# Performance work log

Hardware: AMD Instinct MI355X
Metric: run time of the kernel (lower is better)

The kernel has to match this reference:

```python
import jax, jax.numpy as jnp
import numpy as np

N_NODES = 50000


def setup_inputs() -> dict:
    key = jax.random.key(0)
    k1, k2, k3, k4 = jax.random.split(key, 4)
    in_c, hid = 256, 128
    x = jax.random.normal(k1, (N_NODES, in_c), dtype=jnp.float32)
    edge_index = jax.random.randint(k2, (2, 800000), 0, N_NODES, dtype=jnp.int32)
    # GCNConv weight (glorot) and bias
    W_conv = jax.random.normal(k3, (in_c, hid), dtype=jnp.float32) * (1.0 / np.sqrt(in_c))
    b_conv = jnp.zeros((hid,), dtype=jnp.float32)
    # Final Linear (xavier_uniform per reset_parameters)
    limit = np.sqrt(6.0 / (hid + in_c))
    W_lin = jax.random.uniform(k4, (hid, in_c), dtype=jnp.float32, minval=-limit, maxval=limit)
    b_lin = jnp.zeros((in_c,), dtype=jnp.float32)
    return {"x": x, "edge_index": edge_index, "W_conv": W_conv, "b_conv": b_conv,
            "W_lin": W_lin, "b_lin": b_lin}


def _gcn_conv(x, edge_index, W, b):
    n = x.shape[0]
    # add self-loops (standard GCN normalization)
    loop = jnp.arange(n, dtype=edge_index.dtype)
    src = jnp.concatenate([edge_index[0], loop])
    dst = jnp.concatenate([edge_index[1], loop])
    # transform first (in_c -> hid) so the edge gather moves the smaller dim
    h = x @ W  # [N, hid]
    deg = jax.ops.segment_sum(jnp.ones_like(dst, dtype=h.dtype), dst, num_segments=n)
    dinv = jnp.where(deg > 0, jax.lax.rsqrt(deg), 0.0)
    norm = dinv[src] * dinv[dst]  # [E+N]
    msg = h[src] * norm[:, None]  # [E+N, hid]
    out = jax.ops.segment_sum(msg, dst, num_segments=n)
    return out + b


def reference(x, edge_index, W_conv, b_conv, W_lin, b_lin):
    h = _gcn_conv(x, edge_index, W_conv, b_conv)  # [N, hid]
    # dropout p=0.0 -> identity
    return h @ W_lin + b_lin  # [N, in_c]
```

## Files before the change

kernel.cpp:

```cpp
#include <hip/hip_runtime.h>
#include <hip/hip_fp16.h>


#define N_NODES 50000
#define N_EDGES 800000
#define IN_C 256
#define HID 128
#define SCAN_BLOCKS ((N_NODES + 255) / 256)
#define GEMM_MBLK ((N_NODES + 63) / 64)

#define OFF_H    0UL
#define OFF_CONV 12800000UL
#define OFF_DEG  25600000UL
#define OFF_RP   25800000UL
#define OFF_DINV 26000064UL
#define OFF_RANK 26200064UL
#define OFF_REC  27800064UL
#define OFF_BSUM 31000064UL
#define OFF_WT1  31001088UL
#define OFF_WT2  31066624UL

typedef __attribute__((ext_vector_type(8))) short bf16x8;
typedef __attribute__((ext_vector_type(4))) float f32x4;

__device__ __forceinline__ ushort f2bf(float x) {
    unsigned u = __float_as_uint(x);
    u += 0x7fffu + ((u >> 16) & 1u);
    return (ushort)(u >> 16);
}

__global__ void deg_kernel(const int* __restrict__ dst, int* __restrict__ deg,
                           ushort* __restrict__ rank, int e) {
    int i = blockIdx.x * blockDim.x + threadIdx.x;
    if (i < e) rank[i] = (ushort)atomicAdd(&deg[dst[i]], 1);
}

__global__ __launch_bounds__(256) void scan_blocks_kernel(
    const int* __restrict__ deg, int* __restrict__ row_ptr,
    int* __restrict__ bsums, int n)
{
    __shared__ int tmp[256];
    int tid = threadIdx.x;
    int i = blockIdx.x * 256 + tid;
    int v = (i < n) ? deg[i] : 0;
    int orig = v;
    tmp[tid] = v;
    __syncthreads();
    #pragma unroll
    for (int off = 1; off < 256; off <<= 1) {
        int t = (tid >= off) ? tmp[tid - off] : 0;
        __syncthreads();
        tmp[tid] += t;
        __syncthreads();
    }
    if (i < n) row_ptr[i] = tmp[tid] - orig;
    if (tid == 255) bsums[blockIdx.x] = tmp[255];
}

__global__ __launch_bounds__(256) void scan_sums_kernel(int* __restrict__ bsums, int nb) {
    __shared__ int tmp[256];
    int tid = threadIdx.x;
    int v = (tid < nb) ? bsums[tid] : 0;
    int orig = v;
    tmp[tid] = v;
    __syncthreads();
    #pragma unroll
    for (int off = 1; off < 256; off <<= 1) {
        int t = (tid >= off) ? tmp[tid - off] : 0;
        __syncthreads();
        tmp[tid] += t;
        __syncthreads();
    }
    if (tid < nb) bsums[tid] = tmp[tid] - orig;
}

__global__ __launch_bounds__(256) void finalize_kernel(
    const int* __restrict__ deg, int* __restrict__ row_ptr,
    const int* __restrict__ bsums, float* __restrict__ dinv, int n)
{
    int i = blockIdx.x * 256 + threadIdx.x;
    if (i < n) {
        row_ptr[i] += bsums[blockIdx.x];
        dinv[i] = rsqrtf((float)(deg[i] + 1));
    }
    if (i == 0) row_ptr[n] = N_EDGES;
}

#define BUCKET_BLOCKS 2048
__global__ __launch_bounds__(256) void bucket_kernel(
    const int* __restrict__ src, const int* __restrict__ dst,
    const ushort* __restrict__ rank, const int* __restrict__ row_ptr,
    const float* __restrict__ dinv, unsigned* __restrict__ rec)
{
    int cls = blockIdx.x & 7;
    int blk = blockIdx.x >> 3;
    int lo = cls * (N_NODES / 8);
    int hi = lo + (N_NODES / 8);
    const int CHUNK = (N_EDGES + 255) / 256;
    int e0 = blk * CHUNK;
    int e1 = min(e0 + CHUNK, N_EDGES);
    for (int i = e0 + threadIdx.x; i < e1; i += 256) {
        int d = dst[i];
        if (d >= lo && d < hi) {
            int s = src[i];
            unsigned r = (unsigned)(ushort)s |
                         ((unsigned)__half_as_ushort(__float2half_rn(dinv[s])) << 16);
            rec[row_ptr[d] + rank[i]] = r;
        }
    }
}

__global__ void transpose_w_kernel(const float* __restrict__ W, ushort* __restrict__ Wt,
                                   int K, int N) {
    int i = blockIdx.x * 256 + threadIdx.x;
    if (i < N * K) {
        int n = i / K, k = i % K;
        Wt[i] = f2bf(W[k * N + n]);
    }
}

template <bool A_IS_BF16, bool BF16OUT>
__global__ __launch_bounds__(256) void mfma_gemm_kernel(
    const void* __restrict__ Av, const ushort* __restrict__ Bt,
    const float* __restrict__ bias, void* __restrict__ Cv,
    int M, int N, int K)
{
    constexpr int LDK = 40;
    __shared__ ushort As[64 * LDK];
    __shared__ ushort Bs[128 * LDK];
    int tid = threadIdx.x;
    int wave = tid >> 6, lane = tid & 63;
    int quad = lane >> 4, l16 = lane & 15;
    int wm0 = (wave >> 1) * 32, wn0 = (wave & 1) * 64;
    int bm = blockIdx.x * 64, bn = blockIdx.y * 128;

    f32x4 acc[2][4] = {};

    for (int k0 = 0; k0 < K; k0 += 32) {
        {
            int row = tid >> 2, col = (tid & 3) * 8;
            int grow = bm + row;
            if (A_IS_BF16) {
                bf16x8 v = {};
                if (grow < M)
                    v = *(const bf16x8*)((const ushort*)Av + (size_t)grow * K + k0 + col);
                *(bf16x8*)&As[row * LDK + col] = v;
            } else {
                float4 v0 = make_float4(0.f, 0.f, 0.f, 0.f);
                float4 v1 = make_float4(0.f, 0.f, 0.f, 0.f);
                if (grow < M) {
                    const float* ap = (const float*)Av + (size_t)grow * K + k0 + col;
                    v0 = *(const float4*)ap;
                    v1 = *(const float4*)(ap + 4);
                }
                ushort t[8] = {f2bf(v0.x), f2bf(v0.y), f2bf(v0.z), f2bf(v0.w),
                               f2bf(v1.x), f2bf(v1.y), f2bf(v1.z), f2bf(v1.w)};
                *(bf16x8*)&As[row * LDK + col] = *(bf16x8*)t;
            }
        }
        {
            int ch = tid * 2;
            int n = ch >> 2;
            int kk = (ch & 3) * 8;
            const ushort* bp = Bt + (size_t)(bn + n) * K + k0 + kk;
            *(bf16x8*)&Bs[n * LDK + kk]     = *(const bf16x8*)bp;
            *(bf16x8*)&Bs[n * LDK + kk + 8] = *(const bf16x8*)(bp + 8);
        }
        __syncthreads();
        bf16x8 af[2], bfr[4];
        #pragma unroll
        for (int im = 0; im < 2; ++im)
            af[im] = *(bf16x8*)&As[(wm0 + im * 16 + l16) * LDK + quad * 8];
        #pragma unroll
        for (int in = 0; in < 4; ++in)
            bfr[in] = *(bf16x8*)&Bs[(wn0 + in * 16 + l16) * LDK + quad * 8];
        #pragma unroll
        for (int im = 0; im < 2; ++im)
            #pragma unroll
            for (int in = 0; in < 4; ++in)
                acc[im][in] = __builtin_amdgcn_mfma_f32_16x16x32_bf16(
                    af[im], bfr[in], acc[im][in], 0, 0, 0);
        __syncthreads();
    }
    #pragma unroll
    for (int im = 0; im < 2; ++im) {
        #pragma unroll
        for (int in = 0; in < 4; ++in) {
            int col = bn + wn0 + in * 16 + l16;
            float bval = bias ? bias[col] : 0.f;
            #pragma unroll
            for (int r = 0; r < 4; ++r) {
                int grow = bm + wm0 + im * 16 + quad * 4 + r;
                if (grow < M) {
                    float o = acc[im][in][r] + bval;
                    if (BF16OUT)
                        ((ushort*)Cv)[(size_t)grow * N + col] = f2bf(o);
                    else
                        ((float*)Cv)[(size_t)grow * N + col] = o;
                }
            }
        }
    }
}

__device__ __forceinline__ void acc_edge(float4& acc, unsigned r,
                                         const ushort* __restrict__ hb, int c) {
    unsigned s = r & 0xffffu;
    float w = __half2float(__ushort_as_half((ushort)(r >> 16)));
    uint2 v = *(const uint2*)&hb[(size_t)s * HID + c];
    acc.x += w * __uint_as_float(v.x << 16);
    acc.y += w * __uint_as_float(v.x & 0xffff0000u);
    acc.z += w * __uint_as_float(v.y << 16);
    acc.w += w * __uint_as_float(v.y & 0xffff0000u);
}

__global__ __launch_bounds__(256) void gather_kernel(
    const ushort* __restrict__ hb, const int* __restrict__ row_ptr,
    const unsigned* __restrict__ rec, const float* __restrict__ dinv,
    const float* __restrict__ b_conv, ushort* __restrict__ convb, int n)
{
    int wave = threadIdx.x >> 6;
    int lane = threadIdx.x & 63;
    int d = blockIdx.x * 4 + wave;
    if (d >= n) return;
    int half = lane >> 5;
    int l32 = lane & 31;
    int c = l32 << 2;

    float4 acc = make_float4(0.f, 0.f, 0.f, 0.f);
    int begin = row_ptr[d], end = row_ptr[d + 1];
    int e = begin + half;
    for (; e + 6 < end; e += 8) {
        unsigned r0 = rec[e];
        unsigned r1 = rec[e + 2];
        unsigned r2 = rec[e + 4];
        unsigned r3 = rec[e + 6];
        acc_edge(acc, r0, hb, c);
        acc_edge(acc, r1, hb, c);
        acc_edge(acc, r2, hb, c);
        acc_edge(acc, r3, hb, c);
    }
    for (; e < end; e += 2) {
        unsigned r0 = rec[e];
        acc_edge(acc, r0, hb, c);
    }
    acc.x += __shfl_xor(acc.x, 32);
    acc.y += __shfl_xor(acc.y, 32);
    acc.z += __shfl_xor(acc.z, 32);
    acc.w += __shfl_xor(acc.w, 32);

    if (half == 0) {
        float di = dinv[d];
        uint2 hv = *(const uint2*)&hb[(size_t)d * HID + c];
        acc.x += di * __uint_as_float(hv.x << 16);
        acc.y += di * __uint_as_float(hv.x & 0xffff0000u);
        acc.z += di * __uint_as_float(hv.y << 16);
        acc.w += di * __uint_as_float(hv.y & 0xffff0000u);
        float4 bb = *(const float4*)&b_conv[c];
        float ox = di * acc.x + bb.x;
        float oy = di * acc.y + bb.y;
        float oz = di * acc.z + bb.z;
        float ow = di * acc.w + bb.w;
        uint2 po;
        po.x = ((unsigned)f2bf(oy) << 16) | (unsigned)f2bf(ox);
        po.y = ((unsigned)f2bf(ow) << 16) | (unsigned)f2bf(oz);
        *(uint2*)&convb[(size_t)d * HID + c] = po;
    }
}

extern "C" void kernel_launch(void* const* d_in, const int* in_sizes, int n_in,
                              void* d_out, int out_size, void* d_ws, size_t ws_size,
                              hipStream_t stream) {
    const float* x      = (const float*)d_in[0];
    const int*   ei     = (const int*)d_in[1];
    const float* W_conv = (const float*)d_in[2];
    const float* b_conv = (const float*)d_in[3];
    const float* W_lin  = (const float*)d_in[4];
    const float* b_lin  = (const float*)d_in[5];
    float* out = (float*)d_out;

    char* ws = (char*)d_ws;
    ushort* hb      = (ushort*)(ws + OFF_H);
    ushort* convb   = (ushort*)(ws + OFF_CONV);
    int*    deg     = (int*)(ws + OFF_DEG);
    int*    row_ptr = (int*)(ws + OFF_RP);
    float*  dinv    = (float*)(ws + OFF_DINV);
    ushort* rank    = (ushort*)(ws + OFF_RANK);
    unsigned* rec   = (unsigned*)(ws + OFF_REC);
    int*    bsums   = (int*)(ws + OFF_BSUM);
    ushort* wt_conv = (ushort*)(ws + OFF_WT1);
    ushort* wt_lin  = (ushort*)(ws + OFF_WT2);

    const int* src = ei;
    const int* dst = ei + N_EDGES;

    hipMemsetAsync(deg, 0, 200000, stream);

    deg_kernel<<<(N_EDGES + 255) / 256, 256, 0, stream>>>(dst, deg, rank, N_EDGES);
    scan_blocks_kernel<<<SCAN_BLOCKS, 256, 0, stream>>>(deg, row_ptr, bsums, N_NODES);
    scan_sums_kernel<<<1, 256, 0, stream>>>(bsums, SCAN_BLOCKS);
    finalize_kernel<<<SCAN_BLOCKS, 256, 0, stream>>>(deg, row_ptr, bsums, dinv, N_NODES);
    bucket_kernel<<<BUCKET_BLOCKS, 256, 0, stream>>>(src, dst, rank, row_ptr, dinv, rec);

    transpose_w_kernel<<<(HID * IN_C + 255) / 256, 256, 0, stream>>>(W_conv, wt_conv, IN_C, HID);
    transpose_w_kernel<<<(IN_C * HID + 255) / 256, 256, 0, stream>>>(W_lin, wt_lin, HID, IN_C);

    mfma_gemm_kernel<false, true><<<dim3(GEMM_MBLK, HID / 128), 256, 0, stream>>>(
        x, wt_conv, nullptr, hb, N_NODES, HID, IN_C);

    gather_kernel<<<(N_NODES + 3) / 4, 256, 0, stream>>>(
        hb, row_ptr, rec, dinv, b_conv, convb, N_NODES);

    mfma_gemm_kernel<true, false><<<dim3(GEMM_MBLK, IN_C / 128), 256, 0, stream>>>(
        convb, wt_lin, b_lin, out, N_NODES, IN_C, HID);
}
```

Measured before the change: 235.3 us.

## Fuse prep kernels, merge scan stages, and double GEMM K-tile to 64

Merges the degree-counting atomics with both weight transposes into one prep kernel, and folds the block-sum scan into the finalize kernel so each block rescans the block sums itself. This removes three kernel launches. The GEMM now stages a 64-wide K slice per iteration with a padded LDS stride of 72, which halves the number of loop iterations and barriers at the cost of more LDS and registers. Occupancy may drop from the larger shared tiles, and every finalize block redoes the same small scan.

```diff
diff --git a/kernel.cpp b/kernel.cpp
--- a/kernel.cpp
+++ b/kernel.cpp
@@ -8,6 +8,8 @@
 #define HID 128
 #define SCAN_BLOCKS ((N_NODES + 255) / 256)
 #define GEMM_MBLK ((N_NODES + 63) / 64)
+#define PREP_BLOCKS 1024
+#define LDK 72
 
 #define OFF_H    0UL
 #define OFF_CONV 12800000UL
@@ -29,10 +31,22 @@
     return (ushort)(u >> 16);
 }
 
-__global__ void deg_kernel(const int* __restrict__ dst, int* __restrict__ deg,
-                           ushort* __restrict__ rank, int e) {
-    int i = blockIdx.x * blockDim.x + threadIdx.x;
-    if (i < e) rank[i] = (ushort)atomicAdd(&deg[dst[i]], 1);
+__global__ __launch_bounds__(256) void prep_kernel(
+    const float* __restrict__ Wc, const float* __restrict__ Wl,
+    ushort* __restrict__ wtc, ushort* __restrict__ wtl,
+    const int* __restrict__ dst, ushort* __restrict__ rank, int* __restrict__ deg)
+{
+    int i = blockIdx.x * 256 + threadIdx.x;
+    if (i < HID * IN_C) {
+        int n = i / IN_C, k = i % IN_C;
+        wtc[i] = f2bf(Wc[k * HID + n]);
+    } else if (i < 2 * HID * IN_C) {
+        int j = i - HID * IN_C;
+        int n = j / HID, k = j % HID;
+        wtl[j] = f2bf(Wl[k * IN_C + n]);
+    }
+    for (int e = i; e < N_EDGES; e += PREP_BLOCKS * 256)
+        rank[e] = (ushort)atomicAdd(&deg[dst[e]], 1);
 }
 
 __global__ __launch_bounds__(256) void scan_blocks_kernel(
@@ -57,12 +71,16 @@
     if (tid == 255) bsums[blockIdx.x] = tmp[255];
 }
 
-__global__ __launch_bounds__(256) void scan_sums_kernel(int* __restrict__ bsums, int nb) {
+__global__ __launch_bounds__(256) void finalize2_kernel(
+    const int* __restrict__ deg, int* __restrict__ row_ptr,
+    const int* __restrict__ bsums, float* __restrict__ dinv, int n)
+{
     __shared__ int tmp[256];
+    __shared__ int orig[256];
     int tid = threadIdx.x;
-    int v = (tid < nb) ? bsums[tid] : 0;
-    int orig = v;
+    int v = (tid < SCAN_BLOCKS) ? bsums[tid] : 0;
     tmp[tid] = v;
+    orig[tid] = v;
     __syncthreads();
     #pragma unroll
     for (int off = 1; off < 256; off <<= 1) {
@@ -71,16 +89,10 @@
         tmp[tid] += t;
         __syncthreads();
     }
-    if (tid < nb) bsums[tid] = tmp[tid] - orig;
-}
-
-__global__ __launch_bounds__(256) void finalize_kernel(
-    const int* __restrict__ deg, int* __restrict__ row_ptr,
-    const int* __restrict__ bsums, float* __restrict__ dinv, int n)
-{
-    int i = blockIdx.x * 256 + threadIdx.x;
+    int boff = tmp[blockIdx.x] - orig[blockIdx.x];
+    int i = blockIdx.x * 256 + tid;
     if (i < n) {
-        row_ptr[i] += bsums[blockIdx.x];
+        row_ptr[i] += boff;
         dinv[i] = rsqrtf((float)(deg[i] + 1));
     }
     if (i == 0) row_ptr[n] = N_EDGES;
@@ -110,24 +122,14 @@
     }
 }
 
-__global__ void transpose_w_kernel(const float* __restrict__ W, ushort* __restrict__ Wt,
-                                   int K, int N) {
-    int i = blockIdx.x * 256 + threadIdx.x;
-    if (i < N * K) {
-        int n = i / K, k = i % K;
-        Wt[i] = f2bf(W[k * N + n]);
-    }
-}
-
 template <bool A_IS_BF16, bool BF16OUT>
 __global__ __launch_bounds__(256) void mfma_gemm_kernel(
     const void* __restrict__ Av, const ushort* __restrict__ Bt,
     const float* __restrict__ bias, void* __restrict__ Cv,
     int M, int N, int K)
 {
-    constexpr int LDK = 40;
-    __shared__ ushort As[64 * LDK];
-    __shared__ ushort Bs[128 * LDK];
+    __shared__ __align__(16) ushort As[64 * LDK];
+    __shared__ __align__(16) ushort Bs[128 * LDK];
     int tid = threadIdx.x;
     int wave = tid >> 6, lane = tid & 63;
     int quad = lane >> 4, l16 = lane & 15;
@@ -136,50 +138,66 @@
 
     f32x4 acc[2][4] = {};
 
-    for (int k0 = 0; k0 < K; k0 += 32) {
+    for (int k0 = 0; k0 < K; k0 += 64) {
         {
-            int row = tid >> 2, col = (tid & 3) * 8;
+            int row = tid >> 2, col = (tid & 3) * 16;
             int grow = bm + row;
             if (A_IS_BF16) {
-                bf16x8 v = {};
-                if (grow < M)
-                    v = *(const bf16x8*)((const ushort*)Av + (size_t)grow * K + k0 + col);
-                *(bf16x8*)&As[row * LDK + col] = v;
+                bf16x8 v0 = {}, v1 = {};
+                if (grow < M) {
+                    const ushort* ap = (const ushort*)Av + (size_t)grow * K + k0 + col;
+                    v0 = *(const bf16x8*)ap;
+                    v1 = *(const bf16x8*)(ap + 8);
+                }
+                *(bf16x8*)&As[row * LDK + col]     = v0;
+                *(bf16x8*)&As[row * LDK + col + 8] = v1;
             } else {
-                float4 v0 = make_float4(0.f, 0.f, 0.f, 0.f);
-                float4 v1 = make_float4(0.f, 0.f, 0.f, 0.f);
+                float4 v0 = {}, v1 = {}, v2 = {}, v3 = {};
                 if (grow < M) {
                     const float* ap = (const float*)Av + (size_t)grow * K + k0 + col;
                     v0 = *(const float4*)ap;
                     v1 = *(const float4*)(ap + 4);
+                    v2 = *(const float4*)(ap + 8);
+                    v3 = *(const float4*)(ap + 12);
                 }
-                ushort t[8] = {f2bf(v0.x), f2bf(v0.y), f2bf(v0.z), f2bf(v0.w),
-                               f2bf(v1.x), f2bf(v1.y), f2bf(v1.z), f2bf(v1.w)};
-                *(bf16x8*)&As[row * LDK + col] = *(bf16x8*)t;
+                ushort t0[8] = {f2bf(v0.x), f2bf(v0.y), f2bf(v0.z), f2bf(v0.w),
+                                f2bf(v1.x), f2bf(v1.y), f2bf(v1.z), f2bf(v1.w)};
+                ushort t1[8] = {f2bf(v2.x), f2bf(v2.y), f2bf(v2.z), f2bf(v2.w),
+                                f2bf(v3.x), f2bf(v3.y), f2bf(v3.z), f2bf(v3.w)};
+                *(bf16x8*)&As[row * LDK + col]     = *(bf16x8*)t0;
+                *(bf16x8*)&As[row * LDK + col + 8] = *(bf16x8*)t1;
             }
         }
         {
-            int ch = tid * 2;
-            int n = ch >> 2;
-            int kk = (ch & 3) * 8;
+            int n = tid >> 1;
+            int kk = (tid & 1) * 32;
             const ushort* bp = Bt + (size_t)(bn + n) * K + k0 + kk;
-            *(bf16x8*)&Bs[n * LDK + kk]     = *(const bf16x8*)bp;
-            *(bf16x8*)&Bs[n * LDK + kk + 8] = *(const bf16x8*)(bp + 8);
+            *(bf16x8*)&Bs[n * LDK + kk]      = *(const bf16x8*)bp;
+            *(bf16x8*)&Bs[n * LDK + kk + 8]  = *(const bf16x8*)(bp + 8);
+            *(bf16x8*)&Bs[n * LDK + kk + 16] = *(const bf16x8*)(bp + 16);
+            *(bf16x8*)&Bs[n * LDK + kk + 24] = *(const bf16x8*)(bp + 24);
         }
         __syncthreads();
-        bf16x8 af[2], bfr[4];
-        #pragma unroll
-        for (int im = 0; im < 2; ++im)
-            af[im] = *(bf16x8*)&As[(wm0 + im * 16 + l16) * LDK + quad * 8];
-        #pragma unroll
-        for (int in = 0; in < 4; ++in)
-            bfr[in] = *(bf16x8*)&Bs[(wn0 + in * 16 + l16) * LDK + quad * 8];
+        bf16x8 af[2][2], bfr[4][2];
         #pragma unroll
         for (int im = 0; im < 2; ++im)
             #pragma unroll
-            for (int in = 0; in < 4; ++in)
+            for (int kh = 0; kh < 2; ++kh)
+                af[im][kh] = *(bf16x8*)&As[(wm0 + im * 16 + l16) * LDK + kh * 32 + quad * 8];
+        #pragma unroll
+        for (int in = 0; in < 4; ++in)
+            #pragma unroll
+            for (int kh = 0; kh < 2; ++kh)
+                bfr[in][kh] = *(bf16x8*)&Bs[(wn0 + in * 16 + l16) * LDK + kh * 32 + quad * 8];
+        #pragma unroll
+        for (int im = 0; im < 2; ++im)
+            #pragma unroll
+            for (int in = 0; in < 4; ++in) {
                 acc[im][in] = __builtin_amdgcn_mfma_f32_16x16x32_bf16(
-                    af[im], bfr[in], acc[im][in], 0, 0, 0);
+                    af[im][0], bfr[in][0], acc[im][in], 0, 0, 0);
+                acc[im][in] = __builtin_amdgcn_mfma_f32_16x16x32_bf16(
+                    af[im][1], bfr[in][1], acc[im][in], 0, 0, 0);
+            }
         __syncthreads();
     }
     #pragma unroll
@@ -296,14 +314,11 @@
 
     hipMemsetAsync(deg, 0, 200000, stream);
 
-    deg_kernel<<<(N_EDGES + 255) / 256, 256, 0, stream>>>(dst, deg, rank, N_EDGES);
+    prep_kernel<<<PREP_BLOCKS, 256, 0, stream>>>(W_conv, W_lin, wt_conv, wt_lin,
+                                                 dst, rank, deg);
     scan_blocks_kernel<<<SCAN_BLOCKS, 256, 0, stream>>>(deg, row_ptr, bsums, N_NODES);
-    scan_sums_kernel<<<1, 256, 0, stream>>>(bsums, SCAN_BLOCKS);
-    finalize_kernel<<<SCAN_BLOCKS, 256, 0, stream>>>(deg, row_ptr, bsums, dinv, N_NODES);
+    finalize2_kernel<<<SCAN_BLOCKS, 256, 0, stream>>>(deg, row_ptr, bsums, dinv, N_NODES);
     bucket_kernel<<<BUCKET_BLOCKS, 256, 0, stream>>>(src, dst, rank, row_ptr, dinv, rec);
-
-    transpose_w_kernel<<<(HID * IN_C + 255) / 256, 256, 0, stream>>>(W_conv, wt_conv, IN_C, HID);
-    transpose_w_kernel<<<(IN_C * HID + 255) / 256, 256, 0, stream>>>(W_lin, wt_lin, HID, IN_C);
 
     mfma_gemm_kernel<false, true><<<dim3(GEMM_MBLK, HID / 128), 256, 0, stream>>>(
         x, wt_conv, nullptr, hb, N_NODES, HID, IN_C);
```

Result: faster. 230.5 us (-2.1%).
